# Optimization experiments

Hardware: AMD Instinct MI355X
Metric: run time of the kernel (lower is better)

The kernel has to match this reference:

```python
import jax, jax.numpy as jnp
import numpy as np

B, T, E, H, V, C, L = 32, 512, 512, 512, 50000, 32, 2


def _lstm_dir(x, Wih, Whh, bih, bhh, reverse):
    # x: (B,T,in). Precompute the big input GEMM once; scan only does h @ Whh^T.
    xw = jnp.einsum('bti,gi->btg', x, Wih) + bih + bhh  # (B,T,4H)
    Hd = Whh.shape[1]
    Bd = x.shape[0]

    def step(carry, xt):
        h, c = carry
        g = xt + h @ Whh.T
        i, f, gg, o = jnp.split(g, 4, axis=-1)  # torch gate order i,f,g,o
        c = jax.nn.sigmoid(f) * c + jax.nn.sigmoid(i) * jnp.tanh(gg)
        h = jax.nn.sigmoid(o) * jnp.tanh(c)
        return (h, c), h

    init = (jnp.zeros((Bd, Hd), x.dtype), jnp.zeros((Bd, Hd), x.dtype))
    _, hs = jax.lax.scan(step, init, jnp.swapaxes(xw, 0, 1), reverse=reverse)
    return jnp.swapaxes(hs, 0, 1)  # (B,T,H), time-aligned for both directions


def setup_inputs() -> dict:
    key = jax.random.key(0)
    keys = jax.random.split(key, 40)

    def u(k, shape, scale):
        return jax.random.uniform(k, shape, jnp.float32, -scale, scale)

    s = 1.0 / np.sqrt(H)
    inp = {
        'x': jax.random.randint(keys[0], (B, T), 0, V),
        'truth': jax.random.uniform(keys[1], (B, T, 1), jnp.float32),
        'teacher_forcing': 1,
        'emb': jax.random.normal(keys[2], (V, E), jnp.float32),
    }
    ki = 3
    for l in range(L):
        insz = E if l == 0 else 2 * H
        for d in ('f', 'b'):
            inp[f'Wih{l}{d}'] = u(keys[ki], (4 * H, insz), s); ki += 1
            inp[f'Whh{l}{d}'] = u(keys[ki], (4 * H, H), s); ki += 1
            inp[f'bih{l}{d}'] = u(keys[ki], (4 * H,), s); ki += 1
            inp[f'bhh{l}{d}'] = u(keys[ki], (4 * H,), s); ki += 1
    sc = 1.0 / np.sqrt(2 * H + 1)
    inp['Wc'] = u(keys[ki], (C, 2 * H + 1), sc); ki += 1
    inp['bc'] = u(keys[ki], (C,), sc)
    return inp


def reference(x, truth, teacher_forcing, emb,
              Wih0f, Whh0f, bih0f, bhh0f, Wih0b, Whh0b, bih0b, bhh0b,
              Wih1f, Whh1f, bih1f, bhh1f, Wih1b, Whh1b, bih1b, bhh1b,
              Wc, bc):
    h = emb[x]  # (B,T,E)
    layer_params = [
        ((Wih0f, Whh0f, bih0f, bhh0f), (Wih0b, Whh0b, bih0b, bhh0b)),
        ((Wih1f, Whh1f, bih1f, bhh1f), (Wih1b, Whh1b, bih1b, bhh1b)),
    ]
    for pf, pb in layer_params:
        out_f = _lstm_dir(h, *pf, reverse=False)
        out_b = _lstm_dir(h, *pb, reverse=True)
        h = jnp.concatenate([out_f, out_b], axis=-1)  # (B,T,2H)
    # past feature: zeros at t=0; truth[:, t-1] when teacher forcing, else zeros
    zero0 = jnp.zeros((h.shape[0], 1, 1), h.dtype)
    if teacher_forcing:
        past = jnp.concatenate([zero0, truth[:, :-1, :]], axis=1)  # (B,T,1)
    else:
        past = jnp.zeros((h.shape[0], h.shape[1], 1), h.dtype)
    feat = jnp.concatenate([past, h], axis=-1)  # (B,T,2H+1)
    logits = jnp.einsum('btf,cf->btc', feat, Wc) + bc
    y = jax.nn.log_softmax(logits, axis=-1)  # softmax over classes (intended math)
    return jnp.swapaxes(y, 1, 2)  # (B, classes, T)
```

## Files before the change

### kernel.cpp

```cpp
#include <hip/hip_runtime.h>


#define BB 32
#define TT 512
#define EE 512
#define HH 512
#define NG 2048
#define CC 32

typedef __attribute__((ext_vector_type(8))) short short8v;
typedef __attribute__((ext_vector_type(4))) float float4v;
typedef unsigned long long u64;

__device__ __forceinline__ float bf2f(unsigned short u) {
    return __uint_as_float(((unsigned)u) << 16);
}
__device__ __forceinline__ float bf_lo(unsigned u) { return __uint_as_float(u << 16); }
__device__ __forceinline__ float bf_hi(unsigned u) { return __uint_as_float(u & 0xffff0000u); }
__device__ __forceinline__ unsigned short f2bf(float f) {
    unsigned u = __float_as_uint(f);
    u += 0x7fffu + ((u >> 16) & 1u);
    return (unsigned short)(u >> 16);
}
__device__ __forceinline__ unsigned pk2(float a, float b) {
    return (unsigned)f2bf(a) | ((unsigned)f2bf(b) << 16);
}
__device__ __forceinline__ float fast_sigmoid(float x) {
    return 1.f / (1.f + __expf(-x));
}
__device__ __forceinline__ float fast_tanh(float x) {
    x = fminf(fmaxf(x, -15.f), 15.f);
    float e = __expf(2.f * x);
    return (e - 1.f) / (e + 1.f);
}

__global__ __launch_bounds__(256)
void embed_k(const int* __restrict__ x, const float* __restrict__ emb,
             unsigned short* __restrict__ h0) {
    int idx = blockIdx.x * 256 + threadIdx.x;
    int row = idx >> 7;
    int c4  = idx & 127;
    int tok = x[row];
    float4 v = *(const float4*)(emb + ((size_t)tok << 9) + (c4 << 2));
    ushort4 o;
    o.x = f2bf(v.x); o.y = f2bf(v.y); o.z = f2bf(v.z); o.w = f2bf(v.w);
    *(ushort4*)(h0 + ((size_t)row << 9) + (c4 << 2)) = o;
}

__global__ __launch_bounds__(512)
void gemm_xw(const unsigned short* __restrict__ A, const float* __restrict__ Bw,
             const float* __restrict__ bih, const float* __restrict__ bhh,
             unsigned short* __restrict__ Cp, int M, int K) {
    __shared__ __align__(16) unsigned char As[128 * 128];
    __shared__ __align__(16) unsigned char Bs[128 * 128];
    const int bn = blockIdx.x & 15, bm = blockIdx.x >> 4;
    const int tid = threadIdx.x;
    const int wv = tid >> 6, lane = tid & 63;
    const int wr = wv >> 2, wc = wv & 3;
    const int srow = tid >> 2, skc = (tid & 3) * 16;
    const unsigned sswz = (srow & 7) << 4;
    const int fr = lane & 15, fkb = (lane >> 4) * 16;

    float4v acc[4][2];
#pragma unroll
    for (int i = 0; i < 4; ++i) { acc[i][0] = (float4v)(0.f); acc[i][1] = (float4v)(0.f); }

    const unsigned short* arow_p = A + (size_t)(bm * 128 + srow) * K + skc;
    const float* brow_p = Bw + (size_t)(bn * 128 + srow) * K + skc;
    unsigned char* const as_row = As + srow * 128;
    unsigned char* const bs_row = Bs + srow * 128;
    const int sb0 = skc * 2;

    for (int k0 = 0; k0 < K; k0 += 64) {
        uint4 a0 = *(const uint4*)(arow_p + k0);
        uint4 a1 = *(const uint4*)(arow_p + k0 + 8);
        float4 b0 = *(const float4*)(brow_p + k0);
        float4 b1 = *(const float4*)(brow_p + k0 + 4);
        float4 b2 = *(const float4*)(brow_p + k0 + 8);
        float4 b3 = *(const float4*)(brow_p + k0 + 12);
        *(uint4*)(as_row + ((sb0     ) ^ sswz)) = a0;
        *(uint4*)(as_row + ((sb0 + 16) ^ sswz)) = a1;
        uint4 bp0 = make_uint4(pk2(b0.x, b0.y), pk2(b0.z, b0.w), pk2(b1.x, b1.y), pk2(b1.z, b1.w));
        uint4 bp1 = make_uint4(pk2(b2.x, b2.y), pk2(b2.z, b2.w), pk2(b3.x, b3.y), pk2(b3.z, b3.w));
        *(uint4*)(bs_row + ((sb0     ) ^ sswz)) = bp0;
        *(uint4*)(bs_row + ((sb0 + 16) ^ sswz)) = bp1;
        __syncthreads();

#pragma unroll
        for (int kt = 0; kt < 2; ++kt) {
            const int cb = kt * 64 + fkb;
            short8v af[4], bf[2];
#pragma unroll
            for (int mt = 0; mt < 4; ++mt) {
                const int r = wr * 64 + mt * 16 + fr;
                af[mt] = *(const short8v*)(As + r * 128 + (cb ^ ((r & 7) << 4)));
            }
#pragma unroll
            for (int nt = 0; nt < 2; ++nt) {
                const int r = wc * 32 + nt * 16 + fr;
                bf[nt] = *(const short8v*)(Bs + r * 128 + (cb ^ ((r & 7) << 4)));
            }
#pragma unroll
            for (int mt = 0; mt < 4; ++mt) {
                acc[mt][0] = __builtin_amdgcn_mfma_f32_16x16x32_bf16(af[mt], bf[0], acc[mt][0], 0, 0, 0);
                acc[mt][1] = __builtin_amdgcn_mfma_f32_16x16x32_bf16(af[mt], bf[1], acc[mt][1], 0, 0, 0);
            }
        }
        __syncthreads();
    }

    const int r4 = (lane >> 4) * 4;
#pragma unroll
    for (int nt = 0; nt < 2; ++nt) {
        const int nglob = bn * 128 + wc * 32 + nt * 16 + fr;
        const float bias = bih[nglob] + bhh[nglob];
        const int gate = nglob >> 9;
        const int jbv = (nglob & 511) >> 4;
        const int loc = gate * 16 + (nglob & 15);
#pragma unroll
        for (int mt = 0; mt < 4; ++mt) {
#pragma unroll
            for (int i = 0; i < 4; ++i) {
                const int mglob = bm * 128 + wr * 64 + mt * 16 + r4 + i;
                const int b = mglob >> 9, t = mglob & 511;
                Cp[(((size_t)jbv * 512 + t) * 32 + b) * 64 + loc] =
                    f2bf(acc[mt][nt][i] + bias);
            }
        }
    }
}

__global__ __launch_bounds__(256, 1)
void lstm_scan(const float* __restrict__ WhhF, const float* __restrict__ WhhB,
               const unsigned short* __restrict__ xwF, const unsigned short* __restrict__ xwB,
               unsigned short* __restrict__ outcat,
               u64* __restrict__ h_pp) {
    __shared__ __align__(16) unsigned char hs[16384];
    __shared__ float gsh[4][8][16];
    __shared__ unsigned xsh[2][256];

    const int blk = blockIdx.x;
    const int grp = blk & 7, jb = blk >> 3;
    const int bg = grp & 3, dir = grp >> 2;
    const int tid = threadIdx.x;
    const int wv = tid >> 6, lane = tid & 63;
    const float* Whh = dir ? WhhB : WhhF;
    const unsigned short* xw = dir ? xwB : xwF;
    const int js = jb << 4;

    short8v bw[16];
    {
        const float* wrow = Whh + (size_t)(wv * 512 + js + (lane & 15)) * HH
                            + (lane >> 4) * 8;
#pragma unroll
        for (int kk = 0; kk < 16; ++kk) {
            const float4 f0 = *(const float4*)(wrow + kk * 32);
            const float4 f1 = *(const float4*)(wrow + kk * 32 + 4);
            short8v b;
            b[0] = (short)f2bf(f0.x); b[1] = (short)f2bf(f0.y);
            b[2] = (short)f2bf(f0.z); b[3] = (short)f2bf(f0.w);
            b[4] = (short)f2bf(f1.x); b[5] = (short)f2bf(f1.y);
            b[6] = (short)f2bf(f1.z); b[7] = (short)f2bf(f1.w);
            bw[kk] = b;
        }
    }

    for (int i = tid; i < 8 * 64; i += 256) {
        int r = 8 + (i >> 6), c = i & 63;
        *(uint4*)(hs + r * 1024 + ((c * 16) ^ ((r & 7) << 4))) = make_uint4(0, 0, 0, 0);
    }

    float c_st = 0.f;
    const int srow = tid >> 5, kcol = tid & 31;
    const unsigned swz_w = (srow & 7) << 4;
    const int arow = lane & 15, ag16 = (lane >> 4) * 16;
    const unsigned swz_r = (arow & 7) << 4;
    __syncthreads();

    for (int t = 0; t < TT; ++t) {
        const int tt = dir ? (TT - 1 - t) : t;

        const unsigned xv = *(const unsigned*)(
            xw + (((size_t)jb * 512 + tt) * 32 + bg * 8) * 64 + 2 * tid);

        {
            const u64* hsrc =
                h_pp + ((size_t)((t & 3) * 2 + dir) * BB + bg * 8 + srow) * 256;
            const unsigned sq = (unsigned)t;
            u64 v0, v1, v2, v3, v4, v5, v6, v7;
            for (;;) {
                v0 = __hip_atomic_load(hsrc + kcol,       __ATOMIC_RELAXED, __HIP_MEMORY_SCOPE_AGENT);
                v1 = __hip_atomic_load(hsrc + kcol + 32,  __ATOMIC_RELAXED, __HIP_MEMORY_SCOPE_AGENT);
                v2 = __hip_atomic_load(hsrc + kcol + 64,  __ATOMIC_RELAXED, __HIP_MEMORY_SCOPE_AGENT);
                v3 = __hip_atomic_load(hsrc + kcol + 96,  __ATOMIC_RELAXED, __HIP_MEMORY_SCOPE_AGENT);
                v4 = __hip_atomic_load(hsrc + kcol + 128, __ATOMIC_RELAXED, __HIP_MEMORY_SCOPE_AGENT);
                v5 = __hip_atomic_load(hsrc + kcol + 160, __ATOMIC_RELAXED, __HIP_MEMORY_SCOPE_AGENT);
                v6 = __hip_atomic_load(hsrc + kcol + 192, __ATOMIC_RELAXED, __HIP_MEMORY_SCOPE_AGENT);
                v7 = __hip_atomic_load(hsrc + kcol + 224, __ATOMIC_RELAXED, __HIP_MEMORY_SCOPE_AGENT);
                unsigned ok = ((unsigned)(v0 >> 32) == sq) & ((unsigned)(v1 >> 32) == sq)
                            & ((unsigned)(v2 >> 32) == sq) & ((unsigned)(v3 >> 32) == sq)
                            & ((unsigned)(v4 >> 32) == sq) & ((unsigned)(v5 >> 32) == sq)
                            & ((unsigned)(v6 >> 32) == sq) & ((unsigned)(v7 >> 32) == sq);
                if (ok) break;
                __builtin_amdgcn_s_sleep(1);
            }
            xsh[t & 1][tid] = xv;
            unsigned char* hrow = hs + srow * 1024;
            *(unsigned*)(hrow + ((4 * kcol +   0) ^ swz_w)) = (unsigned)v0;
            *(unsigned*)(hrow + ((4 * kcol + 128) ^ swz_w)) = (unsigned)v1;
            *(unsigned*)(hrow + ((4 * kcol + 256) ^ swz_w)) = (unsigned)v2;
            *(unsigned*)(hrow + ((4 * kcol + 384) ^ swz_w)) = (unsigned)v3;
            *(unsigned*)(hrow + ((4 * kcol + 512) ^ swz_w)) = (unsigned)v4;
            *(unsigned*)(hrow + ((4 * kcol + 640) ^ swz_w)) = (unsigned)v5;
            *(unsigned*)(hrow + ((4 * kcol + 768) ^ swz_w)) = (unsigned)v6;
            *(unsigned*)(hrow + ((4 * kcol + 896) ^ swz_w)) = (unsigned)v7;
        }
        __syncthreads();

        {
            float4v a0 = (float4v)(0.0f), a1 = (float4v)(0.0f);
#pragma unroll
            for (int kk = 0; kk < 16; kk += 2) {
                short8v af0 = *(const short8v*)(hs + arow * 1024 +
                                  (((kk * 64) + ag16) ^ swz_r));
                short8v af1 = *(const short8v*)(hs + arow * 1024 +
                                  ((((kk + 1) * 64) + ag16) ^ swz_r));
                a0 = __builtin_amdgcn_mfma_f32_16x16x32_bf16(af0, bw[kk], a0, 0, 0, 0);
                a1 = __builtin_amdgcn_mfma_f32_16x16x32_bf16(af1, bw[kk + 1], a1, 0, 0, 0);
            }
            if (lane < 32) {
#pragma unroll
                for (int reg = 0; reg < 4; ++reg) {
                    gsh[wv][(lane >> 4) * 4 + reg][lane & 15] = a0[reg] + a1[reg];
                }
            }
        }
        __syncthreads();

        if (tid < 128) {
            const int bl = tid >> 4, jj = tid & 15;
            const unsigned short* xp = (const unsigned short*)xsh[t & 1];
            const int vb = bl * 64 + jj;
            float gi = gsh[0][bl][jj] + bf2f(xp[vb]);
            float gf = gsh[1][bl][jj] + bf2f(xp[vb + 16]);
            float gg = gsh[2][bl][jj] + bf2f(xp[vb + 32]);
            float go = gsh[3][bl][jj] + bf2f(xp[vb + 48]);
            float si = fast_sigmoid(gi);
            float sf = fast_sigmoid(gf);
            float so = fast_sigmoid(go);
            c_st = sf * c_st + si * fast_tanh(gg);
            float hv = so * fast_tanh(c_st);
            const unsigned short hb16 = f2bf(hv);
            const int b_glob = bg * 8 + bl;
            unsigned hv32 = hb16;
            unsigned other = (unsigned)__shfl_xor((int)hv32, 1);
            if (!(tid & 1)) {
                u64 pkt = ((u64)(unsigned)(t + 1) << 32) | (u64)(hv32 | (other << 16));
                __hip_atomic_store(
                    &h_pp[((size_t)(((t + 1) & 3) * 2 + dir) * BB + b_glob) * 256
                          + jb * 8 + (jj >> 1)],
                    pkt, __ATOMIC_RELAXED, __HIP_MEMORY_SCOPE_AGENT);
            }
            outcat[((size_t)b_glob * TT + tt) * 1024 + dir * HH + js + jj] = hb16;
        }
    }
}

__global__ __launch_bounds__(256)
void classifier_k(const unsigned short* __restrict__ hcat, const float* __restrict__ truth,
                  const int* __restrict__ tf, const float* __restrict__ Wc,
                  const float* __restrict__ bc, float* __restrict__ out) {
    __shared__ float feat[8][1024];
    __shared__ float featp[8];
    const int tid = threadIdx.x;
    const int bt0 = blockIdx.x * 8;
    for (int i = tid; i < 8 * 128; i += 256) {
        int bl = i >> 7, ch = i & 127;
        uint4 u = *(const uint4*)(hcat + (size_t)(bt0 + bl) * 1024 + ch * 8);
        *(float4*)&feat[bl][ch * 8] = make_float4(bf_lo(u.x), bf_hi(u.x), bf_lo(u.y), bf_hi(u.y));
        *(float4*)&feat[bl][ch * 8 + 4] = make_float4(bf_lo(u.z), bf_hi(u.z), bf_lo(u.w), bf_hi(u.w));
    }
    if (tid < 8) {
        int bt = bt0 + tid;
        int t = bt & 511;
        featp[tid] = (t > 0 && tf[0] != 0) ? truth[bt - 1] : 0.f;
    }
    __syncthreads();
    const int bl = tid >> 5, c = tid & 31;
    const int bt = bt0 + bl;
    float acc = featp[bl] * Wc[c * 1025] + bc[c];
    const float* w = Wc + c * 1025 + 1;
    for (int f4 = 0; f4 < 256; ++f4) {
        const float4 fv = *(const float4*)&feat[bl][f4 * 4];
        acc = fmaf(fv.x, w[f4 * 4 + 0],
              fmaf(fv.y, w[f4 * 4 + 1],
              fmaf(fv.z, w[f4 * 4 + 2],
              fmaf(fv.w, w[f4 * 4 + 3], acc))));
    }
    float m = acc;
#pragma unroll
    for (int mk = 16; mk; mk >>= 1) m = fmaxf(m, __shfl_xor(m, mk));
    float e = expf(acc - m);
    float s = e;
#pragma unroll
    for (int mk = 16; mk; mk >>= 1) s += __shfl_xor(s, mk);
    float lse = m + logf(s);
    int b = bt >> 9, t = bt & 511;
    out[((size_t)b * CC + c) * TT + t] = acc - lse;
}

extern "C" void kernel_launch(void* const* d_in, const int* in_sizes, int n_in,
                              void* d_out, int out_size, void* d_ws, size_t ws_size,
                              hipStream_t stream) {
    const int* x = (const int*)d_in[0];
    const float* truth = (const float*)d_in[1];
    const int* tf = (const int*)d_in[2];
    const float* emb = (const float*)d_in[3];
    const float* Wih0f = (const float*)d_in[4];
    const float* Whh0f = (const float*)d_in[5];
    const float* bih0f = (const float*)d_in[6];
    const float* bhh0f = (const float*)d_in[7];
    const float* Wih0b = (const float*)d_in[8];
    const float* Whh0b = (const float*)d_in[9];
    const float* bih0b = (const float*)d_in[10];
    const float* bhh0b = (const float*)d_in[11];
    const float* Wih1f = (const float*)d_in[12];
    const float* Whh1f = (const float*)d_in[13];
    const float* bih1f = (const float*)d_in[14];
    const float* bhh1f = (const float*)d_in[15];
    const float* Wih1b = (const float*)d_in[16];
    const float* Whh1b = (const float*)d_in[17];
    const float* bih1b = (const float*)d_in[18];
    const float* bhh1b = (const float*)d_in[19];
    const float* Wc = (const float*)d_in[20];
    const float* bc = (const float*)d_in[21];
    float* out = (float*)d_out;

    const size_t off_h0  = 0;
    const size_t off_xwf = 16777216;
    const size_t off_xwb = off_xwf + 67108864;
    const size_t off_hc1 = off_xwb + 67108864;
    const size_t off_hc2 = off_hc1 + 33554432;
    const size_t off_hpp = off_hc2 + 33554432;
    const size_t need = off_hpp + 524288;
    if (ws_size < need) return;

    char* ws = (char*)d_ws;
    unsigned short* h0  = (unsigned short*)(ws + off_h0);
    unsigned short* xwf = (unsigned short*)(ws + off_xwf);
    unsigned short* xwb = (unsigned short*)(ws + off_xwb);
    unsigned short* hc1 = (unsigned short*)(ws + off_hc1);
    unsigned short* hc2 = (unsigned short*)(ws + off_hc2);
    u64*            hpp = (u64*)(ws + off_hpp);

    embed_k<<<8192, 256, 0, stream>>>(x, emb, h0);

    gemm_xw<<<2048, 512, 0, stream>>>(h0, Wih0f, bih0f, bhh0f, xwf, BB * TT, EE);
    gemm_xw<<<2048, 512, 0, stream>>>(h0, Wih0b, bih0b, bhh0b, xwb, BB * TT, EE);
    (void)hipMemsetAsync(ws + off_hpp, 0, 524288, stream);
    lstm_scan<<<256, 256, 0, stream>>>(Whh0f, Whh0b, xwf, xwb, hc1, hpp);

    gemm_xw<<<2048, 512, 0, stream>>>(hc1, Wih1f, bih1f, bhh1f, xwf, BB * TT, 1024);
    gemm_xw<<<2048, 512, 0, stream>>>(hc1, Wih1b, bih1b, bhh1b, xwb, BB * TT, 1024);
    (void)hipMemsetAsync(ws + off_hpp, 0, 524288, stream);
    lstm_scan<<<256, 256, 0, stream>>>(Whh1f, Whh1b, xwf, xwb, hc2, hpp);

    classifier_k<<<2048, 256, 0, stream>>>(hc2, truth, tf, Wc, bc, out);
}
```

Measured before the change: 3.161 ms.

## Halve LSTM scan blocks by giving each block 32 hidden units with 512 threads

The persistent recurrent scan kernel now runs 128 blocks of 512 threads instead of 256 blocks of 256, each block covering 32 hidden columns (two 16-column chunks per gate). With fewer blocks there are fewer participants in the per-step cross-block handoff of h through global memory. The h poll is also spread over more threads, each thread issuing fewer loads, and the spin loop now reloads only the entries that are still stale. In exchange each block does twice the MFMA and gate work per step, so every step may take longer inside the block.

```diff
diff --git a/kernel.cpp b/kernel.cpp
--- a/kernel.cpp
+++ b/kernel.cpp
@@ -130,27 +130,28 @@
     }
 }
 
-__global__ __launch_bounds__(256, 1)
+__global__ __launch_bounds__(512, 1)
 void lstm_scan(const float* __restrict__ WhhF, const float* __restrict__ WhhB,
                const unsigned short* __restrict__ xwF, const unsigned short* __restrict__ xwB,
                unsigned short* __restrict__ outcat,
                u64* __restrict__ h_pp) {
     __shared__ __align__(16) unsigned char hs[16384];
-    __shared__ float gsh[4][8][16];
-    __shared__ unsigned xsh[2][256];
+    __shared__ float gsh[8][8][16];
+    __shared__ unsigned xsh[2][2][256];
 
     const int blk = blockIdx.x;
-    const int grp = blk & 7, jb = blk >> 3;
+    const int grp = blk & 7, jbb = blk >> 3;
     const int bg = grp & 3, dir = grp >> 2;
     const int tid = threadIdx.x;
     const int wv = tid >> 6, lane = tid & 63;
     const float* Whh = dir ? WhhB : WhhF;
     const unsigned short* xw = dir ? xwB : xwF;
-    const int js = jb << 4;
+    const int js = jbb << 5;
 
     short8v bw[16];
     {
-        const float* wrow = Whh + (size_t)(wv * 512 + js + (lane & 15)) * HH
+        const int g = wv >> 1, ch = wv & 1;
+        const float* wrow = Whh + (size_t)(g * 512 + js + ch * 16 + (lane & 15)) * HH
                             + (lane >> 4) * 8;
 #pragma unroll
         for (int kk = 0; kk < 16; ++kk) {
@@ -165,55 +166,50 @@
         }
     }
 
-    for (int i = tid; i < 8 * 64; i += 256) {
-        int r = 8 + (i >> 6), c = i & 63;
+    {
+        int r = 8 + (tid >> 6), c = tid & 63;
         *(uint4*)(hs + r * 1024 + ((c * 16) ^ ((r & 7) << 4))) = make_uint4(0, 0, 0, 0);
     }
 
     float c_st = 0.f;
-    const int srow = tid >> 5, kcol = tid & 31;
+    const int srow = wv, kcol = lane;
     const unsigned swz_w = (srow & 7) << 4;
     const int arow = lane & 15, ag16 = (lane >> 4) * 16;
     const unsigned swz_r = (arow & 7) << 4;
+    const int xc = tid >> 8, xi = tid & 255;
     __syncthreads();
 
     for (int t = 0; t < TT; ++t) {
         const int tt = dir ? (TT - 1 - t) : t;
 
         const unsigned xv = *(const unsigned*)(
-            xw + (((size_t)jb * 512 + tt) * 32 + bg * 8) * 64 + 2 * tid);
+            xw + (((size_t)(2 * jbb + xc) * 512 + tt) * 32 + bg * 8) * 64 + 2 * xi);
 
         {
             const u64* hsrc =
                 h_pp + ((size_t)((t & 3) * 2 + dir) * BB + bg * 8 + srow) * 256;
             const unsigned sq = (unsigned)t;
-            u64 v0, v1, v2, v3, v4, v5, v6, v7;
-            for (;;) {
-                v0 = __hip_atomic_load(hsrc + kcol,       __ATOMIC_RELAXED, __HIP_MEMORY_SCOPE_AGENT);
-                v1 = __hip_atomic_load(hsrc + kcol + 32,  __ATOMIC_RELAXED, __HIP_MEMORY_SCOPE_AGENT);
-                v2 = __hip_atomic_load(hsrc + kcol + 64,  __ATOMIC_RELAXED, __HIP_MEMORY_SCOPE_AGENT);
-                v3 = __hip_atomic_load(hsrc + kcol + 96,  __ATOMIC_RELAXED, __HIP_MEMORY_SCOPE_AGENT);
-                v4 = __hip_atomic_load(hsrc + kcol + 128, __ATOMIC_RELAXED, __HIP_MEMORY_SCOPE_AGENT);
-                v5 = __hip_atomic_load(hsrc + kcol + 160, __ATOMIC_RELAXED, __HIP_MEMORY_SCOPE_AGENT);
-                v6 = __hip_atomic_load(hsrc + kcol + 192, __ATOMIC_RELAXED, __HIP_MEMORY_SCOPE_AGENT);
-                v7 = __hip_atomic_load(hsrc + kcol + 224, __ATOMIC_RELAXED, __HIP_MEMORY_SCOPE_AGENT);
-                unsigned ok = ((unsigned)(v0 >> 32) == sq) & ((unsigned)(v1 >> 32) == sq)
-                            & ((unsigned)(v2 >> 32) == sq) & ((unsigned)(v3 >> 32) == sq)
-                            & ((unsigned)(v4 >> 32) == sq) & ((unsigned)(v5 >> 32) == sq)
-                            & ((unsigned)(v6 >> 32) == sq) & ((unsigned)(v7 >> 32) == sq);
-                if (ok) break;
+            u64 v0 = __hip_atomic_load(hsrc + kcol,       __ATOMIC_RELAXED, __HIP_MEMORY_SCOPE_AGENT);
+            u64 v1 = __hip_atomic_load(hsrc + kcol + 64,  __ATOMIC_RELAXED, __HIP_MEMORY_SCOPE_AGENT);
+            u64 v2 = __hip_atomic_load(hsrc + kcol + 128, __ATOMIC_RELAXED, __HIP_MEMORY_SCOPE_AGENT);
+            u64 v3 = __hip_atomic_load(hsrc + kcol + 192, __ATOMIC_RELAXED, __HIP_MEMORY_SCOPE_AGENT);
+            bool k0 = (unsigned)(v0 >> 32) == sq;
+            bool k1 = (unsigned)(v1 >> 32) == sq;
+            bool k2 = (unsigned)(v2 >> 32) == sq;
+            bool k3 = (unsigned)(v3 >> 32) == sq;
+            while (!(k0 && k1 && k2 && k3)) {
                 __builtin_amdgcn_s_sleep(1);
-            }
-            xsh[t & 1][tid] = xv;
+                if (!k0) { v0 = __hip_atomic_load(hsrc + kcol,       __ATOMIC_RELAXED, __HIP_MEMORY_SCOPE_AGENT); k0 = (unsigned)(v0 >> 32) == sq; }
+                if (!k1) { v1 = __hip_atomic_load(hsrc + kcol + 64,  __ATOMIC_RELAXED, __HIP_MEMORY_SCOPE_AGENT); k1 = (unsigned)(v1 >> 32) == sq; }
+                if (!k2) { v2 = __hip_atomic_load(hsrc + kcol + 128, __ATOMIC_RELAXED, __HIP_MEMORY_SCOPE_AGENT); k2 = (unsigned)(v2 >> 32) == sq; }
+                if (!k3) { v3 = __hip_atomic_load(hsrc + kcol + 192, __ATOMIC_RELAXED, __HIP_MEMORY_SCOPE_AGENT); k3 = (unsigned)(v3 >> 32) == sq; }
+            }
+            xsh[t & 1][xc][xi] = xv;
             unsigned char* hrow = hs + srow * 1024;
             *(unsigned*)(hrow + ((4 * kcol +   0) ^ swz_w)) = (unsigned)v0;
-            *(unsigned*)(hrow + ((4 * kcol + 128) ^ swz_w)) = (unsigned)v1;
-            *(unsigned*)(hrow + ((4 * kcol + 256) ^ swz_w)) = (unsigned)v2;
-            *(unsigned*)(hrow + ((4 * kcol + 384) ^ swz_w)) = (unsigned)v3;
-            *(unsigned*)(hrow + ((4 * kcol + 512) ^ swz_w)) = (unsigned)v4;
-            *(unsigned*)(hrow + ((4 * kcol + 640) ^ swz_w)) = (unsigned)v5;
-            *(unsigned*)(hrow + ((4 * kcol + 768) ^ swz_w)) = (unsigned)v6;
-            *(unsigned*)(hrow + ((4 * kcol + 896) ^ swz_w)) = (unsigned)v7;
+            *(unsigned*)(hrow + ((4 * kcol + 256) ^ swz_w)) = (unsigned)v1;
+            *(unsigned*)(hrow + ((4 * kcol + 512) ^ swz_w)) = (unsigned)v2;
+            *(unsigned*)(hrow + ((4 * kcol + 768) ^ swz_w)) = (unsigned)v3;
         }
         __syncthreads();
 
@@ -237,14 +233,15 @@
         }
         __syncthreads();
 
-        if (tid < 128) {
-            const int bl = tid >> 4, jj = tid & 15;
-            const unsigned short* xp = (const unsigned short*)xsh[t & 1];
-            const int vb = bl * 64 + jj;
-            float gi = gsh[0][bl][jj] + bf2f(xp[vb]);
-            float gf = gsh[1][bl][jj] + bf2f(xp[vb + 16]);
-            float gg = gsh[2][bl][jj] + bf2f(xp[vb + 32]);
-            float go = gsh[3][bl][jj] + bf2f(xp[vb + 48]);
+        if (tid < 256) {
+            const int bl = tid >> 5, jj = tid & 31;
+            const int jh = jj >> 4, jl = jj & 15;
+            const unsigned short* xp = (const unsigned short*)xsh[t & 1][jh];
+            const int vb = bl * 64 + jl;
+            float gi = gsh[jh][bl][jl]     + bf2f(xp[vb]);
+            float gf = gsh[2 + jh][bl][jl] + bf2f(xp[vb + 16]);
+            float gg = gsh[4 + jh][bl][jl] + bf2f(xp[vb + 32]);
+            float go = gsh[6 + jh][bl][jl] + bf2f(xp[vb + 48]);
             float si = fast_sigmoid(gi);
             float sf = fast_sigmoid(gf);
             float so = fast_sigmoid(go);
@@ -258,7 +255,7 @@
                 u64 pkt = ((u64)(unsigned)(t + 1) << 32) | (u64)(hv32 | (other << 16));
                 __hip_atomic_store(
                     &h_pp[((size_t)(((t + 1) & 3) * 2 + dir) * BB + b_glob) * 256
-                          + jb * 8 + (jj >> 1)],
+                          + jbb * 16 + (jj >> 1)],
                     pkt, __ATOMIC_RELAXED, __HIP_MEMORY_SCOPE_AGENT);
             }
             outcat[((size_t)b_glob * TT + tt) * 1024 + dir * HH + js + jj] = hb16;
@@ -358,12 +355,12 @@
     gemm_xw<<<2048, 512, 0, stream>>>(h0, Wih0f, bih0f, bhh0f, xwf, BB * TT, EE);
     gemm_xw<<<2048, 512, 0, stream>>>(h0, Wih0b, bih0b, bhh0b, xwb, BB * TT, EE);
     (void)hipMemsetAsync(ws + off_hpp, 0, 524288, stream);
-    lstm_scan<<<256, 256, 0, stream>>>(Whh0f, Whh0b, xwf, xwb, hc1, hpp);
+    lstm_scan<<<128, 512, 0, stream>>>(Whh0f, Whh0b, xwf, xwb, hc1, hpp);
 
     gemm_xw<<<2048, 512, 0, stream>>>(hc1, Wih1f, bih1f, bhh1f, xwf, BB * TT, 1024);
     gemm_xw<<<2048, 512, 0, stream>>>(hc1, Wih1b, bih1b, bhh1b, xwb, BB * TT, 1024);
     (void)hipMemsetAsync(ws + off_hpp, 0, 524288, stream);
-    lstm_scan<<<256, 256, 0, stream>>>(Whh1f, Whh1b, xwf, xwb, hc2, hpp);
+    lstm_scan<<<128, 512, 0, stream>>>(Whh1f, Whh1b, xwf, xwb, hc2, hpp);
 
     classifier_k<<<2048, 256, 0, stream>>>(hc2, truth, tf, Wc, bc, out);
 }
```

Measured after the change: 3.281 ms. +3.8%, slower.
